# Kernel tuning notes

Hardware: AMD Instinct MI355X
Metric: run time of the kernel (lower is better)

The kernel has to match this reference:

```python
import jax, jax.numpy as jnp
import numpy as np
import math

H = 64
W = 64
POS_DIM = 64          # (enc_out*9) // patch_length**2
PL = 3                # patch_length
RPL = 3               # reference_patch_length -> 36 offsets
CENTER = (PL * PL) // 2  # 4
NOFF = (2 * RPL) ** 2    # 36


def _unfold3(feat):
    # torch F.unfold(feat, 3, padding=1).view(B, C*9, H, W): channel-major, then 3x3 kernel offsets
    B, C, h, w = feat.shape
    p = jnp.pad(feat, ((0, 0), (0, 0), (1, 1), (1, 1)))
    shifts = [p[:, :, i:i + h, j:j + w] for i in range(3) for j in range(3)]
    return jnp.stack(shifts, axis=2).reshape(B, C * 9, h, w)


def _sinu(rel_pair):
    # pos_enc_sinu_2d_for_point, vectorized: rel_pair [..., 2] -> [..., POS_DIM]
    half = POS_DIM // 2
    div = jnp.exp(jnp.arange(0.0, half, 2.0) * (-(math.log(10000.0) / half)))  # [half/2]
    a = rel_pair[..., 0:1] * div   # [..., half/2]
    b = rel_pair[..., 1:2] * div
    pa = jnp.stack([jnp.sin(a), jnp.cos(a)], axis=-1).reshape(*a.shape[:-1], half)  # interleaved sin/cos
    pb = jnp.stack([jnp.sin(b), jnp.cos(b)], axis=-1).reshape(*b.shape[:-1], half)
    return jnp.concatenate([pa, pb], axis=-1)


def _mlp(x, ws, bs):
    n = len(ws)
    for i in range(n):
        x = x @ ws[i] + bs[i]
        if i < n - 1:
            x = jax.nn.relu(x)
    return x


def _forward(inp, coord, cell, enc_w, enc_b, w0, b0, w1, b1, w2, b2, w3, b3, w4, b4):
    # encoder: 3x3 conv, stride 1, same padding
    feat = jax.lax.conv_general_dilated(inp, enc_w, (1, 1), 'SAME',
                                        dimension_numbers=('NCHW', 'OIHW', 'NCHW'))
    feat = feat + enc_b[None, :, None, None]
    feat = _unfold3(feat)  # [B, C*9, H, W]
    B, Cf, h, w = feat.shape
    Q = coord.shape[1]
    D = coord.shape[-1]  # 18
    rx = 1.0 / h  # 2/h/2
    ry = 1.0 / w
    eps = 1e-6

    offs = jnp.array([v for v in range(-RPL, RPL + 1) if v != 0], jnp.float32)  # [6]
    vx = jnp.repeat(offs, offs.shape[0])  # outer loop over vx -> [36]
    vy = jnp.tile(offs, offs.shape[0])
    even = (jnp.arange(D) % 2 == 0)
    shift = jnp.where(even[None, :], vx[:, None] * rx, vy[:, None] * ry) + eps  # [36, D]

    coord_ = coord[None] + shift[:, None, None, :]  # [36,B,Q,D]
    cc = jnp.clip(coord_[..., 2 * CENTER:2 * CENTER + 2], -1 + 1e-6, 1 - 1e-6)  # center coord [36,B,Q,2]
    # nearest grid_sample, align_corners=False: unnormalize then round
    iy = jnp.clip(jnp.round(((cc[..., 0] + 1) * h - 1) / 2), 0, h - 1).astype(jnp.int32)
    ix = jnp.clip(jnp.round(((cc[..., 1] + 1) * w - 1) / 2), 0, w - 1).astype(jnp.int32)

    flat = feat.transpose(0, 2, 3, 1).reshape(B, h * w, Cf)  # [B,HW,Cf]
    lin = iy * w + ix  # [36,B,Q]
    q_feat = flat[jnp.arange(B)[None, :, None], lin]  # [36,B,Q,Cf]

    # feat_coord at nearest pixel (make_coord cell centers)
    q_coord = jnp.stack([-1.0 + (2.0 * iy.astype(coord.dtype) + 1.0) / h,
                         -1.0 + (2.0 * ix.astype(coord.dtype) + 1.0) / w], axis=-1)  # [36,B,Q,2]

    rel = coord[None] - jnp.tile(q_coord, (1, 1, 1, PL * PL))  # [36,B,Q,18]
    # faithful to source: even indices scaled by h THEN by w; odd indices untouched
    scale = jnp.where(even, float(h) * float(w), 1.0)
    rel = rel * scale

    sinu = _sinu(rel.reshape(NOFF, B, Q, PL * PL, 2)).reshape(NOFF, B, Q, PL * PL * POS_DIM)
    x = q_feat + sinu

    rel_cell = cell * jnp.array([float(h), float(w)], dtype=cell.dtype)  # [B,Q,2]
    x = jnp.concatenate([x, jnp.broadcast_to(rel_cell[None], (NOFF,) + cell.shape)], axis=-1)

    pred = _mlp(x, [w0, w1, w2, w3, w4], [b0, b1, b2, b3, b4])  # [36,B,Q,27]

    area = jnp.abs(rel[..., 0] * rel[..., 1]) + 1e-9  # [36,B,Q]
    tot = area.sum(axis=0)
    perm = np.arange(NOFF)
    perm[[0, 1, 2, 3]] = [3, 2, 1, 0]  # local_ensemble area swap
    area = area[perm]
    return (pred * (area / tot)[..., None]).sum(axis=0)  # [B,Q,27]


def setup_inputs() -> dict:
    key = jax.random.key(0)
    ks = jax.random.split(key, 16)
    B, Q = 2, 2048
    inp = jax.random.normal(ks[0], (B, 3, H, W), jnp.float32)
    coord = jax.random.uniform(ks[1], (B, Q, PL * PL * 2), jnp.float32, minval=-1.0, maxval=1.0)
    cell = jnp.full((B, Q, 2), 2.0 / 192.0, jnp.float32)
    enc_w = jax.random.normal(ks[2], (64, 3, 3, 3), jnp.float32) * 0.05
    enc_b = jnp.zeros((64,), jnp.float32)
    dims = [578, 256, 256, 256, 256, 27]
    params = {}
    for i in range(5):
        fi, fo = dims[i], dims[i + 1]
        s = 1.0 / np.sqrt(fi)
        params['w%d' % i] = jax.random.uniform(ks[3 + 2 * i], (fi, fo), jnp.float32, minval=-s, maxval=s)
        params['b%d' % i] = jax.random.uniform(ks[4 + 2 * i], (fo,), jnp.float32, minval=-s, maxval=s)
    return dict(inp=inp, coord=coord, cell=cell, enc_w=enc_w, enc_b=enc_b, **params)


def reference(inp, coord, cell, enc_w, enc_b, w0, b0, w1, b1, w2, b2, w3, b3, w4, b4):
    return _forward(inp, coord, cell, enc_w, enc_b, w0, b0, w1, b1, w2, b2, w3, b3, w4, b4)
```

## Files before the change

kernel.cpp:

```cpp
#include <hip/hip_runtime.h>
#include <math.h>

typedef _Float16 f16;
typedef f16 f16x8 __attribute__((ext_vector_type(8)));
typedef f16 f16x2 __attribute__((ext_vector_type(2)));
typedef float f32x4 __attribute__((ext_vector_type(4)));

#define BB 2
#define QQ 2048
#define CF 576
#define NOFF 36
#define NBQ (BB*QQ)
#define NROWS (NOFF*NBQ)
#define FEAT_ELEMS (BB*66*66*64)
#define MROWS 48
#define NWG (NROWS/MROWS)
#define PITCHB 640

__global__ __launch_bounds__(256) void k_conv(const float* __restrict__ inp,
                                              const float* __restrict__ ew,
                                              const float* __restrict__ eb,
                                              f16* __restrict__ feat) {
    int idx = blockIdx.x * 256 + threadIdx.x;
    if (idx >= FEAT_ELEMS) return;
    int c = idx & 63;
    int t = idx >> 6;
    int x = t % 66; t /= 66;
    int y = t % 66;
    int b = t / 66;
    float v = 0.f;
    if (y >= 1 && y <= 64 && x >= 1 && x <= 64) {
        int yr = y - 1, xr = x - 1;
        v = eb[c];
        #pragma unroll
        for (int i = 0; i < 3; ++i)
            #pragma unroll
            for (int ky = 0; ky < 3; ++ky) {
                int yy = yr + ky - 1;
                if (yy < 0 || yy > 63) continue;
                #pragma unroll
                for (int kx = 0; kx < 3; ++kx) {
                    int xx = xr + kx - 1;
                    if (xx < 0 || xx > 63) continue;
                    v = fmaf(inp[((b*3 + i)*64 + yy)*64 + xx],
                             ew[((c*3 + i)*3 + ky)*3 + kx], v);
                }
            }
    }
    feat[idx] = (f16)v;
}

__global__ __launch_bounds__(256) void k_wcvt(const float* __restrict__ w0,
                                              const float* __restrict__ w1,
                                              const float* __restrict__ w2,
                                              const float* __restrict__ w3,
                                              const float* __restrict__ w4,
                                              f16* __restrict__ wt0, f16* __restrict__ wt1,
                                              f16* __restrict__ wt2, f16* __restrict__ wt3,
                                              f16* __restrict__ wt4) {
    int i = blockIdx.x * 256 + threadIdx.x;
    if (i < 19*256*32) {
        int kk = i & 31, col = (i >> 5) & 255, ks = i >> 13;
        int k = ks*32 + kk;
        wt0[i] = (f16)((k < 578) ? w0[k*256 + col] : 0.f);
        return;
    }
    i -= 19*256*32;
    if (i < 3*65536) {
        int l = i >> 16, j = i & 65535;
        int kk = j & 31, col = (j >> 5) & 255, ks = j >> 13;
        int k = ks*32 + kk;
        const float* w = (l == 0) ? w1 : (l == 1) ? w2 : w3;
        f16* wt = (l == 0) ? wt1 : (l == 1) ? wt2 : wt3;
        wt[j] = (f16)w[k*256 + col];
        return;
    }
    i -= 3*65536;
    if (i < 8192) {
        int kk = i & 31, col = (i >> 5) & 31, ks = i >> 10;
        int k = ks*32 + kk;
        wt4[i] = (f16)((col < 27) ? w4[k*27 + col] : 0.f);
    }
}

__global__ __launch_bounds__(256) void k_prep(const float* __restrict__ coord,
                                              float* __restrict__ qc0w,
                                              float* __restrict__ qc1w,
                                              float* __restrict__ areaw,
                                              int* __restrict__ iposw) {
    int R = blockIdx.x * 256 + threadIdx.x;
    if (R >= NROWS) return;
    int bq = R / 36, n = R - bq*36;
    const float offs[6] = {-3.f, -2.f, -1.f, 1.f, 2.f, 3.f};
    float vx = offs[n / 6];
    float vy = offs[n % 6];
    const float* cp = coord + bq * 18;
    float cc0 = cp[8] + vx * (1.0f/64.0f) + 1e-6f;
    float cc1 = cp[9] + vy * (1.0f/64.0f) + 1e-6f;
    cc0 = fminf(fmaxf(cc0, -1.f + 1e-6f), 1.f - 1e-6f);
    cc1 = fminf(fmaxf(cc1, -1.f + 1e-6f), 1.f - 1e-6f);
    int iy = (int)rintf(((cc0 + 1.f) * 64.f - 1.f) * 0.5f);
    int ix = (int)rintf(((cc1 + 1.f) * 64.f - 1.f) * 0.5f);
    iy = min(max(iy, 0), 63);
    ix = min(max(ix, 0), 63);
    float qc0 = -1.f + (2.f * (float)iy + 1.f) * (1.0f/64.0f);
    float qc1 = -1.f + (2.f * (float)ix + 1.f) * (1.0f/64.0f);
    float rel0 = (cp[0] - qc0) * 4096.f;
    float rel1 = (cp[1] - qc1);
    qc0w[R] = qc0;
    qc1w[R] = qc1;
    areaw[R] = fabsf(rel0 * rel1) + 1e-9f;
    int b = bq >> 11;
    iposw[R] = ((b*66 + iy)*66 + ix) * 64;
}

__global__ __launch_bounds__(256) void k_wgt(const float* __restrict__ areaw,
                                             float* __restrict__ wgtw) {
    int bq = blockIdx.x * 256 + threadIdx.x;
    if (bq >= NBQ) return;
    float a[36];
    float tot = 0.f;
    #pragma unroll
    for (int n = 0; n < 36; ++n) { a[n] = areaw[bq*36 + n]; tot += a[n]; }
    #pragma unroll
    for (int n = 0; n < 36; ++n) {
        int pn = (n < 4) ? 3 - n : n;
        wgtw[bq*36 + n] = a[pn] / tot;
    }
}

template <int COLS2, int JOFF>
__device__ __forceinline__ void buildX(f16* sX, const f16* __restrict__ feat,
                                       const int* s_ipos, const float* s_crd,
                                       const float* s_qc0, const float* s_qc1,
                                       const float* s_cx, const float* s_cy,
                                       const float* s_div, int tid) {
    constexpr int NPAIR = MROWS * COLS2;
    #pragma unroll 2
    for (int p = tid; p < NPAIR; p += 512) {
        int r = p / COLS2;
        int j = JOFF + ((p - r * COLS2) << 1);
        float v0, v1;
        if (j < CF) {
            int c0 = j / 9,  s0 = j  - c0*9;
            int j1 = j + 1;
            int c1 = j1 / 9, s1 = j1 - c1*9;
            int ip = s_ipos[r];
            float f0 = (float)feat[ip + ((s0/3)*66 + (s0 - (s0/3)*3))*64 + c0];
            float f1 = (float)feat[ip + ((s1/3)*66 + (s1 - (s1/3)*3))*64 + c1];
            int d  = j & 63;
            int pl = j >> 6;
            int h2 = d >> 5;
            float qc = h2 ? s_qc1[r] : s_qc0[r];
            float sc = h2 ? 1.f : 4096.f;
            float comp = (s_crd[r*18 + 2*pl + h2] - qc) * sc;
            float arg  = comp * s_div[(d & 31) >> 1];
            float rev = arg * 0.15915494309189535f;
            rev = rev - rintf(rev);
            v0 = f0 + __builtin_amdgcn_sinf(rev);
            v1 = f1 + __builtin_amdgcn_cosf(rev);
        } else if (j == CF) {
            v0 = s_cx[r]; v1 = s_cy[r];
        } else {
            v0 = 0.f; v1 = 0.f;
        }
        uint off = (uint)(r*PITCHB + (j - JOFF)*2);
        off ^= (uint)((r & 7) << 4);
        f16x2 hv = { (f16)v0, (f16)v1 };
        *(f16x2*)((char*)sX + off) = hv;
    }
}

template <int NKS, int NNT, int PITCHC>
__device__ __forceinline__ void gemmT(const f16* sX, const f16* __restrict__ Wt,
                                      int colbase, int lg,
                                      const uint (&abase)[3], uint aswz,
                                      f32x4 (&acc)[3][NNT]) {
    #pragma unroll
    for (int ks = 0; ks < NKS; ++ks) {
        f16x8 a[3], b[NNT];
        #pragma unroll
        for (int nt = 0; nt < NNT; ++nt)
            b[nt] = *(const f16x8*)(Wt + (ks*PITCHC + colbase + nt*16)*32 + lg*8);
        #pragma unroll
        for (int mt = 0; mt < 3; ++mt)
            a[mt] = *(const f16x8*)((const char*)sX + ((abase[mt] + (uint)(ks*64)) ^ aswz));
        #pragma unroll
        for (int mt = 0; mt < 3; ++mt)
            #pragma unroll
            for (int nt = 0; nt < NNT; ++nt)
                acc[mt][nt] = __builtin_amdgcn_mfma_f32_16x16x32_f16(a[mt], b[nt], acc[mt][nt], 0, 0, 0);
    }
}

__global__ __launch_bounds__(512, 2) void k_mlp(
    const float* __restrict__ coord, const float* __restrict__ cellp,
    const f16* __restrict__ feat,
    const float* __restrict__ qc0w, const float* __restrict__ qc1w,
    const float* __restrict__ wgtw, const int* __restrict__ iposw,
    const f16* __restrict__ wt0, const f16* __restrict__ wt1,
    const f16* __restrict__ wt2, const f16* __restrict__ wt3,
    const f16* __restrict__ wt4,
    const float* __restrict__ b0, const float* __restrict__ b1,
    const float* __restrict__ b2, const float* __restrict__ b3,
    const float* __restrict__ b4,
    float* __restrict__ partial)
{
    __shared__ f16 sX[MROWS * 320];
    __shared__ f16 sBB[2][8192];
    __shared__ float s_crd[MROWS * 18];
    __shared__ float s_qc0[MROWS], s_qc1[MROWS], s_cx[MROWS], s_cy[MROWS], s_wgt[MROWS];
    __shared__ int   s_ipos[MROWS];
    __shared__ float s_div[16];

    int tid = threadIdx.x;
    int R0  = blockIdx.x * MROWS;

    if (tid < 16) s_div[tid] = expf((float)(2*tid) * -0.28782313662425575f);
    if (tid < MROWS) {
        int R  = R0 + tid;
        int bq = R / 36;
        s_qc0[tid]  = __builtin_nontemporal_load(&qc0w[R]);
        s_qc1[tid]  = __builtin_nontemporal_load(&qc1w[R]);
        s_wgt[tid]  = __builtin_nontemporal_load(&wgtw[R]);
        s_ipos[tid] = __builtin_nontemporal_load(&iposw[R]);
        s_cx[tid]   = cellp[bq*2 + 0] * 64.f;
        s_cy[tid]   = cellp[bq*2 + 1] * 64.f;
    }
    for (int i = tid; i < MROWS*18; i += 512) {
        int r = i / 18, d = i - r*18;
        s_crd[i] = coord[((R0 + r)/36)*18 + d];
    }

    int lane = tid & 63;
    int wc   = tid >> 6;
    int l15  = lane & 15;
    int lg   = lane >> 4;
    uint aswz = (uint)((lane & 7) << 4);

    uint abase[3];
    #pragma unroll
    for (int mt = 0; mt < 3; ++mt) {
        int row = mt*16 + l15;
        abase[mt] = (uint)(row * PITCHB + lg*16);
    }

    f32x4 acc[3][2];
    auto zacc = [&]() {
        #pragma unroll
        for (int mt = 0; mt < 3; ++mt)
            #pragma unroll
            for (int nt = 0; nt < 2; ++nt)
                #pragma unroll
                for (int i = 0; i < 4; ++i) acc[mt][nt][i] = 0.f;
    };

    auto stage = [&](f16* dst, const f16* __restrict__ Wt, int ks) {
        if (tid < 256) {
            const char* g = (const char*)Wt + (size_t)ks * 16384 + (size_t)tid * 64;
            char* d = (char*)dst + tid * 16;
            #pragma unroll
            for (int i = 0; i < 4; ++i) {
                __builtin_amdgcn_global_load_lds(
                    (const __attribute__((address_space(1))) void*)(g + i*16),
                    (__attribute__((address_space(3))) void*)(d + i*4096),
                    16, 0, 0);
            }
        }
    };

    auto computeK = [&](const f16* sB, int lks) {
        f16x8 a[3], b[2];
        #pragma unroll
        for (int nt = 0; nt < 2; ++nt)
            b[nt] = *(const f16x8*)((const char*)sB + lg*4096 + (wc*32 + nt*16 + l15)*16);
        #pragma unroll
        for (int mt = 0; mt < 3; ++mt)
            a[mt] = *(const f16x8*)((const char*)sX + ((abase[mt] + (uint)(lks*64)) ^ aswz));
        #pragma unroll
        for (int mt = 0; mt < 3; ++mt)
            #pragma unroll
            for (int nt = 0; nt < 2; ++nt)
                acc[mt][nt] = __builtin_amdgcn_mfma_f32_16x16x32_f16(a[mt], b[nt], acc[mt][nt], 0, 0, 0);
    };

    auto runLayer = [&](const f16* __restrict__ Wt, int gksOff, int nks, int lksOff) {
        stage(sBB[0], Wt, gksOff);
        for (int ks = 0; ks < nks; ++ks) {
            __syncthreads();
            if (ks + 1 < nks) stage(sBB[(ks + 1) & 1], Wt, gksOff + ks + 1);
            computeK(sBB[ks & 1], lksOff + ks);
        }
    };

    auto epi = [&](const float* __restrict__ bias) {
        #pragma unroll
        for (int nt = 0; nt < 2; ++nt) {
            int col = wc*32 + nt*16 + l15;
            float bv = bias[col];
            #pragma unroll
            for (int mt = 0; mt < 3; ++mt)
                #pragma unroll
                for (int i = 0; i < 4; ++i) {
                    int row = mt*16 + lg*4 + i;
                    float v = fmaxf(acc[mt][nt][i] + bv, 0.f);
                    uint off = (uint)(row*PITCHB + col*2) ^ (uint)((row & 7) << 4);
                    *(f16*)((char*)sX + off) = (f16)v;
                }
        }
    };

    __syncthreads();

    zacc();
    buildX<160, 0>(sX, feat, s_ipos, s_crd, s_qc0, s_qc1, s_cx, s_cy, s_div, tid);
    runLayer(wt0, 0, 10, 0);
    __syncthreads();
    buildX<144, 320>(sX, feat, s_ipos, s_crd, s_qc0, s_qc1, s_cx, s_cy, s_div, tid);
    runLayer(wt0, 10, 9, 0);
    __syncthreads();
    epi(b0);

    zacc(); runLayer(wt1, 0, 8, 0); __syncthreads(); epi(b1);
    zacc(); runLayer(wt2, 0, 8, 0); __syncthreads(); epi(b2);
    zacc(); runLayer(wt3, 0, 8, 0); __syncthreads(); epi(b3);
    __syncthreads();

    if (wc == 0) {
        f32x4 a4[3][2];
        #pragma unroll
        for (int mt = 0; mt < 3; ++mt)
            #pragma unroll
            for (int nt = 0; nt < 2; ++nt)
                #pragma unroll
                for (int i = 0; i < 4; ++i) a4[mt][nt][i] = 0.f;
        gemmT<8,2,32>(sX, wt4, l15, lg, abase, aswz, a4);
        int split = 36 - (R0 % 36);
        #pragma unroll
        for (int nt = 0; nt < 2; ++nt) {
            int col = nt*16 + l15;
            float bv = (col < 27) ? b4[col] : 0.f;
            float s0 = 0.f, s1 = 0.f;
            #pragma unroll
            for (int mt = 0; mt < 3; ++mt)
                #pragma unroll
                for (int i = 0; i < 4; ++i) {
                    int row = mt*16 + lg*4 + i;
                    float v = (a4[mt][nt][i] + bv) * s_wgt[row];
                    if (row < split) s0 += v; else s1 += v;
                }
            s0 += __shfl_xor(s0, 16, 64);
            s0 += __shfl_xor(s0, 32, 64);
            s1 += __shfl_xor(s1, 16, 64);
            s1 += __shfl_xor(s1, 32, 64);
            if (lg == 0 && col < 27) {
                __builtin_nontemporal_store(s0, &partial[(size_t)blockIdx.x*56 + col]);
                __builtin_nontemporal_store(s1, &partial[(size_t)blockIdx.x*56 + 28 + col]);
            }
        }
    }
}

__global__ __launch_bounds__(256) void k_red(const float* __restrict__ partial,
                                             float* __restrict__ out) {
    int i = blockIdx.x * 256 + threadIdx.x;
    if (i >= NBQ * 27) return;
    int bq = i / 27, col = i - bq*27;
    int r_lo = bq * 36;
    int w0 = r_lo / 48, w1 = (r_lo + 35) / 48;
    float s = 0.f;
    for (int w = w0; w <= w1; ++w) {
        int seg = (bq == (w*48)/36) ? 0 : 1;
        s += __builtin_nontemporal_load(&partial[(size_t)w*56 + seg*28 + col]);
    }
    out[i] = s;
}

extern "C" void kernel_launch(void* const* d_in, const int* in_sizes, int n_in,
                              void* d_out, int out_size, void* d_ws, size_t ws_size,
                              hipStream_t stream) {
    const float* inp   = (const float*)d_in[0];
    const float* coord = (const float*)d_in[1];
    const float* cellp = (const float*)d_in[2];
    const float* enc_w = (const float*)d_in[3];
    const float* enc_b = (const float*)d_in[4];
    const float* w0 = (const float*)d_in[5];
    const float* b0 = (const float*)d_in[6];
    const float* w1 = (const float*)d_in[7];
    const float* b1 = (const float*)d_in[8];
    const float* w2 = (const float*)d_in[9];
    const float* b2 = (const float*)d_in[10];
    const float* w3 = (const float*)d_in[11];
    const float* b3 = (const float*)d_in[12];
    const float* w4 = (const float*)d_in[13];
    const float* b4 = (const float*)d_in[14];
    float* outp = (float*)d_out;

    float* ws    = (float*)d_ws;
    f16*   feat  = (f16*)ws;
    float* qc0w  = (float*)(feat + FEAT_ELEMS);
    float* qc1w  = qc0w + NROWS;
    float* areaw = qc1w + NROWS;
    float* wgtw  = areaw + NROWS;
    int*   iposw = (int*)(wgtw + NROWS);
    float* partial = (float*)(iposw + NROWS);
    f16*   wt0   = (f16*)(partial + (size_t)NWG*56);
    f16*   wt1   = wt0 + 19*256*32;
    f16*   wt2   = wt1 + 65536;
    f16*   wt3   = wt2 + 65536;
    f16*   wt4   = wt3 + 65536;

    k_conv<<<(FEAT_ELEMS + 255)/256, 256, 0, stream>>>(inp, enc_w, enc_b, feat);
    k_wcvt<<<1408, 256, 0, stream>>>(w0, w1, w2, w3, w4, wt0, wt1, wt2, wt3, wt4);
    k_prep<<<NROWS/256, 256, 0, stream>>>(coord, qc0w, qc1w, areaw, iposw);
    k_wgt<<<(NBQ + 255)/256, 256, 0, stream>>>(areaw, wgtw);
    k_mlp<<<NWG, 512, 0, stream>>>(coord, cellp, feat, qc0w, qc1w, wgtw, iposw,
                                   wt0, wt1, wt2, wt3, wt4,
                                   b0, b1, b2, b3, b4, partial);
    k_red<<<(NBQ*27 + 255)/256, 256, 0, stream>>>(partial, outp);
}
```

Measured before the change: 309.2 us.

## Triple-buffer weight staging with manual waitcnt barriers and split layer-0 build

Weight tiles move from a double buffer to a triple buffer. Synchronisation is now explicit vmcnt/lgkmcnt waits plus raw s_barrier and sched barriers instead of __syncthreads, so global-to-LDS weight loads run two k-steps ahead. The X staging pitch shrinks to 512 bytes, and layer 0's input is built in three chunks (128/128/48) to fit, with the next layer's first weight tiles prefetched before the epilogue. Biases are preloaded into registers once. Hand-counted waitcnts are fragile and could cause races if the load counts are off.

```diff
diff --git a/kernel.cpp b/kernel.cpp
--- a/kernel.cpp
+++ b/kernel.cpp
@@ -15,7 +15,7 @@
 #define FEAT_ELEMS (BB*66*66*64)
 #define MROWS 48
 #define NWG (NROWS/MROWS)
-#define PITCHB 640
+#define PITCHB 512
 
 __global__ __launch_bounds__(256) void k_conv(const float* __restrict__ inp,
                                               const float* __restrict__ ew,
@@ -193,6 +193,23 @@
     }
 }
 
+__device__ __forceinline__ void waitv4() {
+    asm volatile("s_waitcnt vmcnt(4)" ::: "memory");
+    __builtin_amdgcn_sched_barrier(0);
+}
+__device__ __forceinline__ void waitv0() {
+    asm volatile("s_waitcnt vmcnt(0)" ::: "memory");
+    __builtin_amdgcn_sched_barrier(0);
+}
+__device__ __forceinline__ void waitlgkm() {
+    asm volatile("s_waitcnt lgkmcnt(0)" ::: "memory");
+    __builtin_amdgcn_sched_barrier(0);
+}
+__device__ __forceinline__ void barrier() {
+    __builtin_amdgcn_s_barrier();
+    __builtin_amdgcn_sched_barrier(0);
+}
+
 __global__ __launch_bounds__(512, 2) void k_mlp(
     const float* __restrict__ coord, const float* __restrict__ cellp,
     const f16* __restrict__ feat,
@@ -206,8 +223,8 @@
     const float* __restrict__ b4,
     float* __restrict__ partial)
 {
-    __shared__ f16 sX[MROWS * 320];
-    __shared__ f16 sBB[2][8192];
+    __shared__ f16 sX[MROWS * 256];
+    __shared__ f16 sBB[3][8192];
     __shared__ float s_crd[MROWS * 18];
     __shared__ float s_qc0[MROWS], s_qc1[MROWS], s_cx[MROWS], s_cy[MROWS], s_wgt[MROWS];
     __shared__ int   s_ipos[MROWS];
@@ -245,6 +262,24 @@
         abase[mt] = (uint)(row * PITCHB + lg*16);
     }
 
+    float bvL[4][2], bv4[2];
+    {
+        const float* Bs[4] = {b0, b1, b2, b3};
+        #pragma unroll
+        for (int L = 0; L < 4; ++L)
+            #pragma unroll
+            for (int nt = 0; nt < 2; ++nt) {
+                bvL[L][nt] = Bs[L][wc*32 + nt*16 + l15];
+                asm volatile("" :: "v"(bvL[L][nt]));
+            }
+        #pragma unroll
+        for (int nt = 0; nt < 2; ++nt) {
+            int col = nt*16 + l15;
+            bv4[nt] = (col < 27) ? b4[col] : 0.f;
+            asm volatile("" :: "v"(bv4[nt]));
+        }
+    }
+
     f32x4 acc[3][2];
     auto zacc = [&]() {
         #pragma unroll
@@ -267,6 +302,7 @@
                     16, 0, 0);
             }
         }
+        __builtin_amdgcn_sched_barrier(0);
     };
 
     auto computeK = [&](const f16* sB, int lks) {
@@ -284,26 +320,16 @@
                 acc[mt][nt] = __builtin_amdgcn_mfma_f32_16x16x32_f16(a[mt], b[nt], acc[mt][nt], 0, 0, 0);
     };
 
-    auto runLayer = [&](const f16* __restrict__ Wt, int gksOff, int nks, int lksOff) {
-        stage(sBB[0], Wt, gksOff);
-        for (int ks = 0; ks < nks; ++ks) {
-            __syncthreads();
-            if (ks + 1 < nks) stage(sBB[(ks + 1) & 1], Wt, gksOff + ks + 1);
-            computeK(sBB[ks & 1], lksOff + ks);
-        }
-    };
-
-    auto epi = [&](const float* __restrict__ bias) {
+    auto epi = [&](const float (&bv)[2]) {
         #pragma unroll
         for (int nt = 0; nt < 2; ++nt) {
             int col = wc*32 + nt*16 + l15;
-            float bv = bias[col];
             #pragma unroll
             for (int mt = 0; mt < 3; ++mt)
                 #pragma unroll
                 for (int i = 0; i < 4; ++i) {
                     int row = mt*16 + lg*4 + i;
-                    float v = fmaxf(acc[mt][nt][i] + bv, 0.f);
+                    float v = fmaxf(acc[mt][nt][i] + bv[nt], 0.f);
                     uint off = (uint)(row*PITCHB + col*2) ^ (uint)((row & 7) << 4);
                     *(f16*)((char*)sX + off) = (f16)v;
                 }
@@ -313,18 +339,60 @@
     __syncthreads();
 
     zacc();
-    buildX<160, 0>(sX, feat, s_ipos, s_crd, s_qc0, s_qc1, s_cx, s_cy, s_div, tid);
-    runLayer(wt0, 0, 10, 0);
-    __syncthreads();
-    buildX<144, 320>(sX, feat, s_ipos, s_crd, s_qc0, s_qc1, s_cx, s_cy, s_div, tid);
-    runLayer(wt0, 10, 9, 0);
-    __syncthreads();
-    epi(b0);
-
-    zacc(); runLayer(wt1, 0, 8, 0); __syncthreads(); epi(b1);
-    zacc(); runLayer(wt2, 0, 8, 0); __syncthreads(); epi(b2);
-    zacc(); runLayer(wt3, 0, 8, 0); __syncthreads(); epi(b3);
-    __syncthreads();
+    buildX<128, 0>(sX, feat, s_ipos, s_crd, s_qc0, s_qc1, s_cx, s_cy, s_div, tid);
+    stage(sBB[0], wt0, 0);
+    stage(sBB[1], wt0, 1);
+    waitlgkm(); barrier();
+    #pragma unroll
+    for (int ks = 0; ks < 8; ++ks) {
+        waitv4();
+        barrier();
+        stage(sBB[(ks + 2) % 3], wt0, ks + 2);
+        computeK(sBB[ks % 3], ks);
+    }
+    barrier();
+    buildX<128, 256>(sX, feat, s_ipos, s_crd, s_qc0, s_qc1, s_cx, s_cy, s_div, tid);
+    waitlgkm(); barrier();
+    #pragma unroll
+    for (int t = 0; t < 8; ++t) {
+        int ks = t + 8;
+        waitv4();
+        barrier();
+        stage(sBB[(ks + 2) % 3], wt0, ks + 2);
+        computeK(sBB[ks % 3], t);
+    }
+    barrier();
+    buildX<48, 512>(sX, feat, s_ipos, s_crd, s_qc0, s_qc1, s_cx, s_cy, s_div, tid);
+    waitlgkm(); barrier();
+    #pragma unroll
+    for (int t = 0; t < 3; ++t) {
+        int ks = t + 16;
+        if (ks + 1 < 19) waitv4(); else waitv0();
+        barrier();
+        if (ks + 2 < 19) stage(sBB[(ks + 2) % 3], wt0, ks + 2);
+        computeK(sBB[ks % 3], t);
+    }
+
+    const f16* Ws[3] = {wt1, wt2, wt3};
+    #pragma unroll
+    for (int L = 0; L < 3; ++L) {
+        barrier();
+        stage(sBB[0], Ws[L], 0);
+        stage(sBB[1], Ws[L], 1);
+        epi(bvL[L]);
+        zacc();
+        waitlgkm(); barrier();
+        #pragma unroll
+        for (int ks = 0; ks < 8; ++ks) {
+            if (ks + 1 < 8) waitv4(); else waitv0();
+            barrier();
+            if (ks + 2 < 8) stage(sBB[(ks + 2) % 3], Ws[L], ks + 2);
+            computeK(sBB[ks % 3], ks);
+        }
+    }
+    barrier();
+    epi(bvL[3]);
+    waitlgkm(); barrier();
 
     if (wc == 0) {
         f32x4 a4[3][2];
@@ -339,14 +407,13 @@
         #pragma unroll
         for (int nt = 0; nt < 2; ++nt) {
             int col = nt*16 + l15;
-            float bv = (col < 27) ? b4[col] : 0.f;
             float s0 = 0.f, s1 = 0.f;
             #pragma unroll
             for (int mt = 0; mt < 3; ++mt)
                 #pragma unroll
                 for (int i = 0; i < 4; ++i) {
                     int row = mt*16 + lg*4 + i;
-                    float v = (a4[mt][nt][i] + bv) * s_wgt[row];
+                    float v = (a4[mt][nt][i] + bv4[nt]) * s_wgt[row];
                     if (row < split) s0 += v; else s1 += v;
                 }
             s0 += __shfl_xor(s0, 16, 64);
```

Measured after the change: 288.9 us. 6.5% less time.
